# Kernel optimization log

Measured on AMD Instinct MI355X. Metric: run time of the kernel, lower is better.

Reference implementation:

```python
import jax, jax.numpy as jnp
import numpy as np
import math

EPS = 1e-6
P_MIN = 1e-3
P_MAX = 10.0
NUM_ITERS = 3
REG = 1.0
K = 64       # num_clusters
D = 128      # cluster_dim
TOKEN = 256  # token_dim
B, N, C = 8, 8192, 512


def _l2norm(t):
    return t / jnp.clip(jnp.linalg.norm(t, axis=-1, keepdims=True), 1e-12)


def _mlp(h, W1, b1, W2, b2):
    # torch Linear: y = h @ W.T + b ; dropout is identity at eval
    return jax.nn.relu(h @ W1.T + b1) @ W2.T + b2


def _log_otp_solver(log_a, log_b, M, num_iters, reg):
    M = M / reg
    u = jnp.zeros_like(log_a)
    v = jnp.zeros_like(log_b)
    for _ in range(num_iters):  # fixed small iteration count
        u = log_a - jax.scipy.special.logsumexp(M + v[:, None, :], axis=2)
        v = log_b - jax.scipy.special.logsumexp(M + u[:, :, None], axis=1)
    return M + u[:, :, None] + v[:, None, :]


def _get_matching_probs(S, dustbin_score, num_iters, reg):
    b, m, n = S.shape
    dust_row = jnp.broadcast_to(dustbin_score, (b, 1, n)).astype(S.dtype)
    S_aug = jnp.concatenate([S, dust_row], axis=1)  # [b, m+1, n]
    norm = -math.log(n + m)
    log_a = jnp.full((m + 1,), norm, dtype=S.dtype).at[-1].add(math.log(n - m))
    log_a = jnp.broadcast_to(log_a, (b, m + 1))
    log_b = jnp.full((b, n), norm, dtype=S.dtype)
    log_P = _log_otp_solver(log_a, log_b, S_aug, num_iters, reg)
    return log_P - norm


def setup_inputs() -> dict:
    key = jax.random.key(0)
    ks = jax.random.split(key, 8)
    x = jax.random.normal(ks[0], (B, N, C), dtype=jnp.float32)

    def lin(k, fin, fout):
        k1, k2 = jax.random.split(k)
        W = 0.02 * jax.random.normal(k1, (fout, fin), dtype=jnp.float32)
        b = 0.02 * jax.random.normal(k2, (fout,), dtype=jnp.float32)
        return W, b

    tW1, tb1 = lin(ks[1], C, 512)
    tW2, tb2 = lin(ks[2], 512, TOKEN)
    cW1, cb1 = lin(ks[3], C, 512)
    cW2, cb2 = lin(ks[4], 512, D)
    sW1, sb1 = lin(ks[5], C, 512)
    sW2, sb2 = lin(ks[6], 512, K)
    # GeM p param init so that softplus(w)+p_min == 3.0
    gem_w = jnp.array([math.log(math.exp(3.0 - P_MIN) - 1.0)], dtype=jnp.float32)
    dust_bin = jnp.array(1.0, dtype=jnp.float32)
    return dict(x=x, gem_w=gem_w, dust_bin=dust_bin,
                tW1=tW1, tb1=tb1, tW2=tW2, tb2=tb2,
                cW1=cW1, cb1=cb1, cW2=cW2, cb2=cb2,
                sW1=sW1, sb1=sb1, sW2=sW2, sb2=sb2)


def reference(x, gem_w, dust_bin,
              tW1, tb1, tW2, tb2,
              cW1, cb1, cW2, cb2,
              sW1, sb1, sW2, sb2):
    # --- GeM pooling: [B, N, C] -> [B, C] ---
    p = jnp.minimum(jax.nn.softplus(gem_w) + P_MIN, P_MAX)  # [1]
    g = jnp.mean(jnp.clip(x.astype(jnp.float32), EPS, None) ** p, axis=1) ** (1.0 / p)
    g = jnp.where(jnp.isfinite(g), g, jnp.zeros_like(g))

    global_token = _mlp(g, tW1, tb1, tW2, tb2)          # [B, TOKEN]
    local = _mlp(x, cW1, cb1, cW2, cb2)                 # [B, N, D]
    scores = _mlp(x, sW1, sb1, sW2, sb2)                # [B, N, K]

    S = scores.transpose(0, 2, 1)                       # [B, K, N]
    log_P = _get_matching_probs(S, dust_bin, NUM_ITERS, REG)  # [B, K+1, N]
    p_mat = jnp.exp(log_P)[:, :-1, :]                   # drop dustbin -> [B, K, N]

    # aggregated[b, d, k] = sum_n local[b, n, d] * p[b, k, n]  (no O(B*D*K*N) blowup)
    agg = jnp.einsum('bnd,bkn->bdk', local, p_mat).reshape(x.shape[0], -1)  # [B, D*K]

    result = jnp.concatenate([_l2norm(global_token), _l2norm(agg)], axis=-1)
    return _l2norm(result)
```

## Files before the change

kernel.cpp:

```cpp
#include <hip/hip_runtime.h>
#include <hip/hip_bf16.h>
#include <math.h>

#define BB   8
#define NN   8192
#define CC   512
#define DD   128
#define KK   64
#define TOK  256
#define MM   (BB*NN)

typedef unsigned short u16;
typedef __attribute__((ext_vector_type(8))) short short8;
typedef __attribute__((ext_vector_type(4))) float floatx4;

struct PtrSz { const void* p[15]; int sz[15]; };

__device__ __forceinline__ float bf2f(u16 v) {
    union { unsigned u; float f; } x; x.u = ((unsigned)v) << 16; return x.f;
}
__device__ __forceinline__ u16 f2bf(float f) {
    union { float f; unsigned u; } x; x.f = f;
    unsigned r = x.u + 0x7fffu + ((x.u >> 16) & 1u);
    return (u16)(r >> 16);
}
__device__ __forceinline__ float nat_exp2(float a) {
    float r; asm("v_exp_f32 %0, %1" : "=v"(r) : "v"(a)); return r;
}
__device__ __forceinline__ float nat_log2(float a) {
    float r; asm("v_log_f32 %0, %1" : "=v"(r) : "v"(a)); return r;
}

__global__ __launch_bounds__(256)
void fill_sentinel(float* __restrict__ out, int n, float val) {
    int i = blockIdx.x*256 + threadIdx.x;
    if (i < n) out[i] = val;
}

__global__ __launch_bounds__(256)
void detect_all(PtrSz ps, int* __restrict__ flags) {
    int i = blockIdx.x;
    const u16* q = (const u16*)ps.p[i];
    int m = ps.sz[i] < 4096 ? ps.sz[i] : 4096;
    __shared__ int cnt;
    if (threadIdx.x == 0) cnt = 0;
    __syncthreads();
    int c = 0;
    for (int j = threadIdx.x; j < m; j += 256) {
        int e = (q[j] >> 7) & 0xFF;
        if (e < 90 || e > 165) c++;
    }
    atomicAdd(&cnt, c);
    __syncthreads();
    if (threadIdx.x == 0) flags[i] = (cnt * 8 > m) ? 1 : 0;
}

#define W_TW1 0
#define W_TB1 262144
#define W_TW2 262656
#define W_TB2 393728
#define W_CW1 393984
#define W_CB1 656128
#define W_CW2 656640
#define W_CB2 722176
#define W_SW1 722304
#define W_SB1 984448
#define W_SW2 984960
#define W_SB2 1017728
#define W_TOTAL 1017792

__global__ __launch_bounds__(256)
void conv_weights(PtrSz ps, const int* __restrict__ flags,
                  u16* __restrict__ wbuf, float* __restrict__ wscal) {
    long gid = (long)blockIdx.x*256 + threadIdx.x;
    if (gid == 0) {
        float vb = bf2f(((const u16*)ps.p[1])[0]);
        float vf = ((const float*)ps.p[1])[0];
        wscal[0] = (fabsf(vb - 2.94694f) < 0.2f) ? vb : vf;
    } else if (gid == 1) {
        float vb = bf2f(((const u16*)ps.p[2])[0]);
        float vf = ((const float*)ps.p[2])[0];
        wscal[1] = (fabsf(vb - 1.0f) < 0.2f) ? vb : vf;
    }
    if (gid >= W_TOTAL) return;
    int idx; long off;
    if      (gid < W_TB1) { idx = 3;  off = W_TW1; }
    else if (gid < W_TW2) { idx = 4;  off = W_TB1; }
    else if (gid < W_TB2) { idx = 5;  off = W_TW2; }
    else if (gid < W_CW1) { idx = 6;  off = W_TB2; }
    else if (gid < W_CB1) { idx = 7;  off = W_CW1; }
    else if (gid < W_CW2) { idx = 8;  off = W_CB1; }
    else if (gid < W_CB2) { idx = 9;  off = W_CW2; }
    else if (gid < W_SW1) { idx = 10; off = W_CB2; }
    else if (gid < W_SB1) { idx = 11; off = W_SW1; }
    else if (gid < W_SW2) { idx = 12; off = W_SB1; }
    else if (gid < W_SB2) { idx = 13; off = W_SW2; }
    else                  { idx = 14; off = W_SB2; }
    long k = gid - off;
    bool f32in = flags[idx] != 0;
    wbuf[gid] = f32in ? f2bf(((const float*)ps.p[idx])[k]) : ((const u16*)ps.p[idx])[k];
}

__global__ __launch_bounds__(256)
void gem_partial(const void* __restrict__ x, const float* __restrict__ wscal,
                 const int* __restrict__ flags, float* __restrict__ gacc) {
    __shared__ float red[4][512];
    int b = blockIdx.x, ny = blockIdx.y;
    int tid  = threadIdx.x;
    int wave = tid >> 6, lane = tid & 63;
    bool f32in = (flags[0] != 0);
    float gw = wscal[0];
    float p  = fminf(log1pf(expf(gw)) + 1e-3f, 10.0f);
    int c0 = lane*8;
    float s[8];
#pragma unroll
    for (int j = 0; j < 8; ++j) s[j] = 0.f;
    size_t base = ((size_t)b*NN + (size_t)ny*64 + wave)*CC + c0;
    if (f32in) {
        const float* xf = (const float*)x;
#pragma unroll 4
        for (int n = 0; n < 64; n += 4) {
            const float* pf = xf + base + (size_t)n*CC;
            float4 x0 = *(const float4*)pf;
            float4 x1 = *(const float4*)(pf + 4);
            float xv[8] = {x0.x,x0.y,x0.z,x0.w,x1.x,x1.y,x1.z,x1.w};
#pragma unroll
            for (int j = 0; j < 8; ++j)
                s[j] += nat_exp2(p * nat_log2(fmaxf(xv[j], 1e-6f)));
        }
    } else {
        const u16* xu = (const u16*)x;
#pragma unroll 4
        for (int n = 0; n < 64; n += 4) {
            short8 v8 = *(const short8*)(xu + base + (size_t)n*CC);
#pragma unroll
            for (int j = 0; j < 8; ++j)
                s[j] += nat_exp2(p * nat_log2(fmaxf(bf2f((u16)v8[j]), 1e-6f)));
        }
    }
#pragma unroll
    for (int j = 0; j < 8; ++j) red[wave][c0 + j] = s[j];
    __syncthreads();
#pragma unroll
    for (int t = 0; t < 2; ++t) {
        int c = tid + t*256;
        float v = red[0][c] + red[1][c] + red[2][c] + red[3][c];
        atomicAdd(&gacc[b*CC + c], v);
    }
}

__global__ __launch_bounds__(256)
void gem_finalize(const float* __restrict__ gacc, const float* __restrict__ wscal,
                  float* __restrict__ g) {
    int i = blockIdx.x*256 + threadIdx.x;
    float gw = wscal[0];
    float p  = fminf(log1pf(expf(gw)) + 1e-3f, 10.0f);
    float m  = gacc[i] / (float)NN;
    float r  = powf(m, 1.0f/p);
    if (!isfinite(r)) r = 0.f;
    g[i] = r;
}

__global__ __launch_bounds__(512)
void token_mlp(const float* __restrict__ g, const u16* __restrict__ wbuf,
               float* __restrict__ t) {
    __shared__ float gs[CC];
    __shared__ float hs[512];
    int b = blockIdx.x, j = threadIdx.x;
    gs[j] = g[b*CC + j];
    __syncthreads();
    float a = bf2f(wbuf[W_TB1 + j]);
    const u16* w = wbuf + W_TW1 + (size_t)j*CC;
    for (int c = 0; c < CC; ++c) a += gs[c]*bf2f(w[c]);
    hs[j] = fmaxf(a, 0.f);
    __syncthreads();
    if (j < TOK) {
        float a2 = bf2f(wbuf[W_TB2 + j]);
        const u16* w2 = wbuf + W_TW2 + (size_t)j*512;
        for (int c = 0; c < 512; ++c) a2 += hs[c]*bf2f(w2[c]);
        t[b*TOK + j] = a2;
    }
}

template<int BN, int MODE, bool RELU, bool ARAW>
__global__ __launch_bounds__(256)
void gemm_bt(const void* __restrict__ A, const u16* __restrict__ W,
             const u16* __restrict__ bias, void* __restrict__ Cout,
             const int* __restrict__ flags, int N, int Ksz,
             size_t a_base, int bidx_ovr) {
    constexpr int WSUB_N = BN/32;
    extern __shared__ char smem[];
    u16* a_lds = (u16*)smem;
    u16* b_lds = (u16*)smem + 128*32;
    const int tid  = threadIdx.x;
    const int wave = tid >> 6, lane = tid & 63;
    const int wm = wave >> 1, wn = wave & 1;
    const int bm0 = blockIdx.x * 128;
    const int bn0 = blockIdx.y * BN;
    const int fr = lane & 15;
    const int fk = (lane >> 4) * 8;
    const bool f32in = ARAW && (flags[0] != 0);

    floatx4 acc[4][WSUB_N];
#pragma unroll
    for (int i = 0; i < 4; ++i)
#pragma unroll
        for (int j = 0; j < WSUB_N; ++j) acc[i][j] = (floatx4){0.f,0.f,0.f,0.f};

    for (int k0 = 0; k0 < Ksz; k0 += 32) {
#pragma unroll
        for (int part = 0; part < 2; ++part) {
            int chunk = part*256 + tid;
            int row = chunk >> 2, kc = (chunk & 3)*8;
            size_t gidx = a_base + (size_t)(bm0 + row)*Ksz + k0 + kc;
            short8 vA;
            if (f32in) {
                const float* pf = (const float*)A + gidx;
                float4 x0 = *(const float4*)pf;
                float4 x1 = *(const float4*)(pf + 4);
                vA[0]=(short)f2bf(x0.x); vA[1]=(short)f2bf(x0.y);
                vA[2]=(short)f2bf(x0.z); vA[3]=(short)f2bf(x0.w);
                vA[4]=(short)f2bf(x1.x); vA[5]=(short)f2bf(x1.y);
                vA[6]=(short)f2bf(x1.z); vA[7]=(short)f2bf(x1.w);
            } else {
                vA = *(const short8*)((const u16*)A + gidx);
            }
            *(short8*)(a_lds + row*32 + kc) = vA;
        }
#pragma unroll
        for (int part = 0; part < BN/64; ++part) {
            int chunk = part*256 + tid;
            int row = chunk >> 2, kc = (chunk & 3)*8;
            short8 vB = *(const short8*)(W + (size_t)(bn0 + row)*Ksz + k0 + kc);
            *(short8*)(b_lds + row*32 + kc) = vB;
        }
        __syncthreads();
        short8 af[4], bfr[WSUB_N];
#pragma unroll
        for (int i = 0; i < 4; ++i)
            af[i] = *(const short8*)(a_lds + (wm*64 + i*16 + fr)*32 + fk);
#pragma unroll
        for (int j = 0; j < WSUB_N; ++j)
            bfr[j] = *(const short8*)(b_lds + (wn*WSUB_N*16 + j*16 + fr)*32 + fk);
#pragma unroll
        for (int i = 0; i < 4; ++i)
#pragma unroll
            for (int j = 0; j < WSUB_N; ++j)
                acc[i][j] = __builtin_amdgcn_mfma_f32_16x16x32_bf16(af[i], bfr[j], acc[i][j], 0, 0, 0);
        __syncthreads();
    }

    if constexpr (MODE == 0) {
        u16* C = (u16*)Cout;
#pragma unroll
        for (int i = 0; i < 4; ++i) {
            int row0 = wm*64 + i*16 + ((lane>>4)<<2);
#pragma unroll
            for (int j = 0; j < WSUB_N; ++j) {
                int col = wn*WSUB_N*16 + j*16 + fr;
                float bb = bf2f(bias[bn0+col]);
#pragma unroll
                for (int r = 0; r < 4; ++r) {
                    float v = acc[i][j][r] + bb;
                    if (RELU) v = fmaxf(v, 0.f);
                    C[(size_t)(bm0+row0+r)*N + (bn0+col)] = f2bf(v);
                }
            }
        }
    } else {
        const int bidx = (bidx_ovr >= 0) ? bidx_ovr : (bm0 >> 13);
        const int nin  = bm0 & 8191;
        if constexpr (MODE == 1) {
            u16* tr = (u16*)smem;
#pragma unroll
            for (int i = 0; i < 4; ++i) {
                int row0 = wm*64 + i*16 + ((lane>>4)<<2);
#pragma unroll
                for (int j = 0; j < WSUB_N; ++j) {
                    int col = wn*WSUB_N*16 + j*16 + fr;
                    float bb = bf2f(bias[bn0+col]);
#pragma unroll
                    for (int r = 0; r < 4; ++r) {
                        float v = acc[i][j][r] + bb;
                        if (RELU) v = fmaxf(v, 0.f);
                        tr[col*128 + row0 + r] = f2bf(v);
                    }
                }
            }
            __syncthreads();
            u16* O = (u16*)Cout;
#pragma unroll
            for (int c = 0; c < (BN*128)/256; ++c) {
                int flat = c*256 + tid;
                int dcol = flat >> 7, rr = flat & 127;
                O[(size_t)(bidx*BN + bn0 + dcol)*NN + nin + rr] = tr[dcol*128 + rr];
            }
        } else {
            float* tr = (float*)smem;
#pragma unroll
            for (int i = 0; i < 4; ++i) {
                int row0 = wm*64 + i*16 + ((lane>>4)<<2);
#pragma unroll
                for (int j = 0; j < WSUB_N; ++j) {
                    int col = wn*WSUB_N*16 + j*16 + fr;
                    float bb = bf2f(bias[bn0+col]);
#pragma unroll
                    for (int r = 0; r < 4; ++r) {
                        float v = acc[i][j][r] + bb;
                        if (RELU) v = fmaxf(v, 0.f);
                        tr[col*128 + row0 + r] = v;
                    }
                }
            }
            __syncthreads();
            float* O = (float*)Cout;
#pragma unroll
            for (int c = 0; c < (BN*128)/256; ++c) {
                int flat = c*256 + tid;
                int dcol = flat >> 7, rr = flat & 127;
                O[(size_t)(bidx*BN + bn0 + dcol)*NN + nin + rr] = tr[dcol*128 + rr];
            }
        }
    }
}

__global__ __launch_bounds__(256)
void sink_u(const float* __restrict__ ST, const float* __restrict__ v,
            const float* __restrict__ wscal, float* __restrict__ u) {
    int m = blockIdx.x, b = blockIdx.y, t = threadIdx.x;
    const float norm = -logf(8256.0f);
    float la = (m == 64) ? norm + logf(8128.0f) : norm;
    float dustf = wscal[1];
    const float* vb = v + (size_t)b*NN;
    float r[32];
    float mx = -1e30f;
    if (m < 64) {
        const float* row = ST + ((size_t)b*64 + m)*NN;
#pragma unroll
        for (int i = 0; i < 32; ++i) { int n = t + i*256; r[i] = row[n] + vb[n]; mx = fmaxf(mx, r[i]); }
    } else {
#pragma unroll
        for (int i = 0; i < 32; ++i) { int n = t + i*256; r[i] = dustf + vb[n]; mx = fmaxf(mx, r[i]); }
    }
#pragma unroll
    for (int off = 32; off; off >>= 1) mx = fmaxf(mx, __shfl_xor(mx, off));
    __shared__ float red[4];
    if ((t & 63) == 0) red[t>>6] = mx;
    __syncthreads();
    mx = fmaxf(fmaxf(red[0], red[1]), fmaxf(red[2], red[3]));
    __syncthreads();
    float s = 0.f;
#pragma unroll
    for (int i = 0; i < 32; ++i) s += expf(r[i] - mx);
#pragma unroll
    for (int off = 32; off; off >>= 1) s += __shfl_xor(s, off);
    if ((t & 63) == 0) red[t>>6] = s;
    __syncthreads();
    s = red[0] + red[1] + red[2] + red[3];
    if (t == 0) u[b*65 + m] = la - (mx + logf(s));
}

__global__ __launch_bounds__(256)
void sink_v(const float* __restrict__ ST, const float* __restrict__ u,
            const float* __restrict__ wscal, float* __restrict__ v) {
    int b = blockIdx.y;
    int n = blockIdx.x*256 + threadIdx.x;
    __shared__ float us[65];
    if (threadIdx.x < 65) us[threadIdx.x] = u[b*65 + threadIdx.x];
    __syncthreads();
    const float norm = -logf(8256.0f);
    float mx = wscal[1] + us[64];
    float s  = 1.0f;
    const float* col = ST + (size_t)b*64*NN + n;
    for (int m = 0; m < 64; ++m) {
        float tv = col[(size_t)m*NN] + us[m];
        float nm = fmaxf(mx, tv);
        s = s*expf(mx - nm) + expf(tv - nm);
        mx = nm;
    }
    v[(size_t)b*NN + n] = norm - (mx + logf(s));
}

__global__ __launch_bounds__(256)
void sink_p(const float* __restrict__ ST, const float* __restrict__ u,
            const float* __restrict__ v, u16* __restrict__ P) {
    int b = blockIdx.y;
    int n = blockIdx.x*256 + threadIdx.x;
    const float norm = -logf(8256.0f);
    float vn = v[(size_t)b*NN + n];
    for (int k = 0; k < 64; ++k) {
        float lp = ST[((size_t)b*64 + k)*NN + n] + u[b*65 + k] + vn - norm;
        P[((size_t)b*64 + k)*NN + n] = f2bf(expf(lp));
    }
}

__global__ __launch_bounds__(256)
void agg_mfma(const u16* __restrict__ localT, const u16* __restrict__ P,
              float* __restrict__ agg) {
    __shared__ u16 a_lds[128*32];
    __shared__ u16 b_lds[64*32];
    int b = blockIdx.y, ns = blockIdx.x;
    int n0 = ns*256;
    const int tid  = threadIdx.x;
    const int wave = tid >> 6, lane = tid & 63;
    const int wm = wave >> 1, wn = wave & 1;
    const int fr = lane & 15, fk = (lane >> 4)*8;

    floatx4 acc[4][2];
#pragma unroll
    for (int i = 0; i < 4; ++i)
#pragma unroll
        for (int j = 0; j < 2; ++j) acc[i][j] = (floatx4){0.f,0.f,0.f,0.f};

    for (int s = 0; s < 8; ++s) {
        int nk = n0 + s*32;
#pragma unroll
        for (int part = 0; part < 2; ++part) {
            int chunk = part*256 + tid;
            int row = chunk >> 2, kc = (chunk & 3)*8;
            short8 vA = *(const short8*)(localT + ((size_t)b*128 + row)*NN + nk + kc);
            *(short8*)(a_lds + row*32 + kc) = vA;
        }
        {
            int row = tid >> 2, kc = (tid & 3)*8;
            short8 vB = *(const short8*)(P + ((size_t)b*64 + row)*NN + nk + kc);
            *(short8*)(b_lds + row*32 + kc) = vB;
        }
        __syncthreads();
        short8 af[4], bfr[2];
#pragma unroll
        for (int i = 0; i < 4; ++i)
            af[i] = *(const short8*)(a_lds + (wm*64 + i*16 + fr)*32 + fk);
#pragma unroll
        for (int j = 0; j < 2; ++j)
            bfr[j] = *(const short8*)(b_lds + (wn*32 + j*16 + fr)*32 + fk);
#pragma unroll
        for (int i = 0; i < 4; ++i)
#pragma unroll
            for (int j = 0; j < 2; ++j)
                acc[i][j] = __builtin_amdgcn_mfma_f32_16x16x32_bf16(af[i], bfr[j], acc[i][j], 0, 0, 0);
        __syncthreads();
    }
#pragma unroll
    for (int i = 0; i < 4; ++i) {
        int d0 = wm*64 + i*16 + ((lane>>4)<<2);
#pragma unroll
        for (int j = 0; j < 2; ++j) {
            int k = wn*32 + j*16 + fr;
#pragma unroll
            for (int r = 0; r < 4; ++r)
                atomicAdd(&agg[(size_t)b*8192 + (d0+r)*64 + k], acc[i][j][r]);
        }
    }
}

__global__ __launch_bounds__(256)
void finalize_out(const float* __restrict__ tg, const float* __restrict__ agg,
                  float* __restrict__ out) {
    int b = blockIdx.x, tid = threadIdx.x;
    float tv = tg[b*TOK + tid];
    float s1 = tv*tv;
    const float* ab = agg + (size_t)b*8192;
    float av[32];
    float s2 = 0.f;
#pragma unroll
    for (int i = 0; i < 32; ++i) { av[i] = ab[tid + i*256]; s2 += av[i]*av[i]; }
#pragma unroll
    for (int off = 32; off; off >>= 1) { s1 += __shfl_xor(s1, off); s2 += __shfl_xor(s2, off); }
    __shared__ float r1[4], r2[4];
    int wave = tid >> 6, lane = tid & 63;
    if (lane == 0) { r1[wave] = s1; r2[wave] = s2; }
    __syncthreads();
    float S1 = r1[0]+r1[1]+r1[2]+r1[3];
    float S2 = r2[0]+r2[1]+r2[2]+r2[3];
    const float rs2 = 1.41421356237f;
    float sc1 = 1.0f/(fmaxf(sqrtf(S1), 1e-12f)*rs2);
    float sc2 = 1.0f/(fmaxf(sqrtf(S2), 1e-12f)*rs2);
    out[(size_t)b*8448 + tid] = tv*sc1;
#pragma unroll
    for (int i = 0; i < 32; ++i)
        out[(size_t)b*8448 + 256 + tid + i*256] = av[i]*sc2;
}

extern "C" void kernel_launch(void* const* d_in, const int* in_sizes, int n_in,
                              void* d_out, int out_size, void* d_ws, size_t ws_size,
                              hipStream_t stream) {
    float* out = (float*)d_out;

    static const int EXP[15] = {33554432,1,1,262144,512,131072,256,
                                262144,512,65536,128,262144,512,32768,64};
    bool ok = (n_in == 15) && (out_size == 67584);
    if (ok) for (int i = 0; i < 15; ++i) ok = ok && (in_sizes[i] == EXP[i]);
    if (!ok) {
        fill_sentinel<<<264, 256, 0, stream>>>(out, out_size, 0.25f);
        return;
    }
    const size_t NEED_BATCH = 52934656ull;
    if (ws_size < NEED_BATCH) {
        fill_sentinel<<<264, 256, 0, stream>>>(out, out_size, 0.5f);
        return;
    }

    const void* x = d_in[0];
    PtrSz ps;
    for (int i = 0; i < 15; ++i) { ps.p[i] = d_in[i]; ps.sz[i] = in_sizes[i]; }

    char* base = (char*)d_ws;
    float* gacc = (float*)(base + 0);
    float* u    = (float*)(base + 16384);
    float* v    = (float*)(base + 18464);
    float* agg  = (float*)(base + 280608);
    const size_t ZERO_BYTES = 542752;
    float* g    = (float*)(base + 542752);
    float* tglb = (float*)(base + 559136);
    int*   flags= (int*)  (base + 567328);
    float* wscal= (float*)(base + 567392);
    u16*   wbuf = (u16*)  (base + 567424);
    float* ST   = (float*)(base + 2603008);
    u16* localT = (u16*)  (base + 19380224);
    u16* P      = (u16*)  (base + 36157440);
    u16* h1     = (u16*)  (base + 44546048);
    const size_t FULL_NEED = 44546048ull + 67108864ull;
    const bool mono = (ws_size >= FULL_NEED);

    hipMemsetAsync(d_ws, 0, ZERO_BYTES, stream);

    detect_all<<<15, 256, 0, stream>>>(ps, flags);
    conv_weights<<<3977, 256, 0, stream>>>(ps, flags, wbuf, wscal);

    gem_partial<<<dim3(BB, 128), 256, 0, stream>>>(x, wscal, flags, gacc);
    gem_finalize<<<16, 256, 0, stream>>>(gacc, wscal, g);
    token_mlp<<<BB, 512, 0, stream>>>(g, wbuf, tglb);

    if (mono) {
        gemm_bt<128, 0, true,  true ><<<dim3(512, 4), 256, 16384, stream>>>(
            x, wbuf + W_CW1, wbuf + W_CB1, h1, flags, 512, 512, 0, -1);
        gemm_bt<128, 1, false, false><<<dim3(512, 1), 256, 32768, stream>>>(
            h1, wbuf + W_CW2, wbuf + W_CB2, localT, flags, 128, 512, 0, -1);
        gemm_bt<128, 0, true,  true ><<<dim3(512, 4), 256, 16384, stream>>>(
            x, wbuf + W_SW1, wbuf + W_SB1, h1, flags, 512, 512, 0, -1);
        gemm_bt< 64, 2, false, false><<<dim3(512, 1), 256, 32768, stream>>>(
            h1, wbuf + W_SW2, wbuf + W_SB2, ST, flags, 64, 512, 0, -1);
    } else {
        for (int b = 0; b < BB; ++b) {
            size_t ab = (size_t)b*NN*CC;
            gemm_bt<128, 0, true,  true ><<<dim3(64, 4), 256, 16384, stream>>>(
                x, wbuf + W_CW1, wbuf + W_CB1, h1, flags, 512, 512, ab, -1);
            gemm_bt<128, 1, false, false><<<dim3(64, 1), 256, 32768, stream>>>(
                h1, wbuf + W_CW2, wbuf + W_CB2, localT, flags, 128, 512, 0, b);
            gemm_bt<128, 0, true,  true ><<<dim3(64, 4), 256, 16384, stream>>>(
                x, wbuf + W_SW1, wbuf + W_SB1, h1, flags, 512, 512, ab, -1);
            gemm_bt< 64, 2, false, false><<<dim3(64, 1), 256, 32768, stream>>>(
                h1, wbuf + W_SW2, wbuf + W_SB2, ST, flags, 64, 512, 0, b);
        }
    }

    for (int it = 0; it < 3; ++it) {
        sink_u<<<dim3(65, BB), 256, 0, stream>>>(ST, v, wscal, u);
        sink_v<<<dim3(32, BB), 256, 0, stream>>>(ST, u, wscal, v);
    }
    sink_p<<<dim3(32, BB), 256, 0, stream>>>(ST, u, v, P);

    agg_mfma<<<dim3(32, BB), 256, 0, stream>>>(localT, P, agg);
    finalize_out<<<BB, 256, 0, stream>>>(tglb, agg, out);
}
```

Before: 562.8 us.

## Use direct global-to-LDS loads and XCD-aware block remapping in GEMM

Replaces the register-staged global loads into LDS for the bf16 A and W tiles with the global_load_lds builtin. This removes the VGPR round trip and the separate ds_write instructions. It also remaps workgroup indices so consecutive tiles land on the same XCD, to improve L2 reuse of shared W and A tiles. The f32 input path still converts through registers, and there is still no double buffering, so latency hiding remains limited.

```diff
diff --git a/kernel.cpp b/kernel.cpp
--- a/kernel.cpp
+++ b/kernel.cpp
@@ -29,6 +29,11 @@
 }
 __device__ __forceinline__ float nat_log2(float a) {
     float r; asm("v_log_f32 %0, %1" : "=v"(r) : "v"(a)); return r;
+}
+__device__ __forceinline__ void gload16(const void* g, void* l) {
+    __builtin_amdgcn_global_load_lds(
+        (const __attribute__((address_space(1))) void*)g,
+        (__attribute__((address_space(3))) void*)l, 16, 0, 0);
 }
 
 __global__ __launch_bounds__(256)
@@ -195,8 +200,21 @@
     const int tid  = threadIdx.x;
     const int wave = tid >> 6, lane = tid & 63;
     const int wm = wave >> 1, wn = wave & 1;
-    const int bm0 = blockIdx.x * 128;
-    const int bn0 = blockIdx.y * BN;
+
+    int bx = blockIdx.x, by = blockIdx.y;
+    {
+        int nbx = gridDim.x, nby = gridDim.y;
+        int nwg = nbx*nby;
+        if ((nwg & 7) == 0) {
+            int lid = bx + by*nbx;
+            int q = nwg >> 3;
+            int t = (lid & 7)*q + (lid >> 3);
+            by = t % nby;
+            bx = t / nby;
+        }
+    }
+    const int bm0 = bx * 128;
+    const int bn0 = by * BN;
     const int fr = lane & 15;
     const int fk = (lane >> 4) * 8;
     const bool f32in = ARAW && (flags[0] != 0);
@@ -208,31 +226,39 @@
         for (int j = 0; j < WSUB_N; ++j) acc[i][j] = (floatx4){0.f,0.f,0.f,0.f};
 
     for (int k0 = 0; k0 < Ksz; k0 += 32) {
-#pragma unroll
-        for (int part = 0; part < 2; ++part) {
-            int chunk = part*256 + tid;
-            int row = chunk >> 2, kc = (chunk & 3)*8;
-            size_t gidx = a_base + (size_t)(bm0 + row)*Ksz + k0 + kc;
-            short8 vA;
-            if (f32in) {
+        if (f32in) {
+#pragma unroll
+            for (int part = 0; part < 2; ++part) {
+                int chunk = part*256 + tid;
+                int row = chunk >> 2, kc = (chunk & 3)*8;
+                size_t gidx = a_base + (size_t)(bm0 + row)*Ksz + k0 + kc;
                 const float* pf = (const float*)A + gidx;
                 float4 x0 = *(const float4*)pf;
                 float4 x1 = *(const float4*)(pf + 4);
+                short8 vA;
                 vA[0]=(short)f2bf(x0.x); vA[1]=(short)f2bf(x0.y);
                 vA[2]=(short)f2bf(x0.z); vA[3]=(short)f2bf(x0.w);
                 vA[4]=(short)f2bf(x1.x); vA[5]=(short)f2bf(x1.y);
                 vA[6]=(short)f2bf(x1.z); vA[7]=(short)f2bf(x1.w);
-            } else {
-                vA = *(const short8*)((const u16*)A + gidx);
-            }
-            *(short8*)(a_lds + row*32 + kc) = vA;
+                *(short8*)(a_lds + row*32 + kc) = vA;
+            }
+        } else {
+#pragma unroll
+            for (int part = 0; part < 2; ++part) {
+                int cb = part*256 + wave*64;
+                int mych = cb + lane;
+                int row = mych >> 2, kc = (mych & 3)*8;
+                gload16((const u16*)A + a_base + (size_t)(bm0 + row)*Ksz + k0 + kc,
+                        a_lds + (size_t)cb*8);
+            }
         }
 #pragma unroll
         for (int part = 0; part < BN/64; ++part) {
-            int chunk = part*256 + tid;
-            int row = chunk >> 2, kc = (chunk & 3)*8;
-            short8 vB = *(const short8*)(W + (size_t)(bn0 + row)*Ksz + k0 + kc);
-            *(short8*)(b_lds + row*32 + kc) = vB;
+            int cb = part*256 + wave*64;
+            int mych = cb + lane;
+            int row = mych >> 2, kc = (mych & 3)*8;
+            gload16(W + (size_t)(bn0 + row)*Ksz + k0 + kc,
+                    b_lds + (size_t)cb*8);
         }
         __syncthreads();
         short8 af[4], bfr[WSUB_N];
```

Result: faster. 513.3 us (-8.8%).
